# Kernel optimization log

Hardware: AMD Instinct MI355X
Metric: run time of the kernel (lower is better)

The kernel has to match this reference:

```python
import jax, jax.numpy as jnp
import numpy as np

N_NODES = 50000
N_EDGES = 600000
D_IN, D_HID, D_OUT = 128, 256, 128


def setup_inputs() -> dict:
    key = jax.random.key(0)
    ks = jax.random.split(key, 8)
    x = jax.random.normal(ks[0], (N_NODES, D_IN), dtype=jnp.float32)
    edge_index = jax.random.randint(ks[1], (2, N_EDGES), 0, N_NODES, dtype=jnp.int64)
    # init_method='uniform' -> edge_weights initialized to ones
    edge_weights = jnp.ones((N_EDGES,), dtype=jnp.float32)
    def lin(k, din, dout):
        s = 1.0 / np.sqrt(din)
        return jax.random.uniform(k, (din, dout), jnp.float32, -s, s)
    W1 = lin(ks[2], D_IN, D_HID)
    b1 = jnp.zeros((D_HID,), jnp.float32)
    W2 = lin(ks[3], D_HID, D_HID)
    b2 = jnp.zeros((D_HID,), jnp.float32)
    W3 = lin(ks[4], D_HID, D_OUT)
    b3 = jnp.zeros((D_OUT,), jnp.float32)
    return {"x": x, "edge_index": edge_index, "edge_weights": edge_weights,
            "W1": W1, "b1": b1, "W2": W2, "b2": b2, "W3": W3, "b3": b3}


def reference(x, edge_index, edge_weights, W1, b1, W2, b2, W3, b3):
    N = x.shape[0]
    # learnable metric: softplus on raw edge weights
    ew = jax.nn.softplus(edge_weights)
    src, dst = edge_index[0], edge_index[1]
    # GCNConv default: add self-loops with weight 1.0
    loop = jnp.arange(N, dtype=edge_index.dtype)
    s = jnp.concatenate([src, loop])
    d = jnp.concatenate([dst, loop])
    w = jnp.concatenate([ew, jnp.ones((N,), ew.dtype)])
    # symmetric degree normalization (gcn_norm); identical edge_weight across layers
    deg = jax.ops.segment_sum(w, d, num_segments=N)
    dinv = jnp.where(deg > 0, jax.lax.rsqrt(deg), jnp.zeros_like(deg))
    norm = dinv[s] * w * dinv[d]  # [E+N]

    def gcn_conv(h, W, b):
        h = h @ W                              # [N, dout]
        msg = h[s] * norm[:, None]             # gather + scale: [E+N, dout]
        out = jax.ops.segment_sum(msg, d, num_segments=N)  # scatter-add
        return out + b

    h = jax.nn.relu(gcn_conv(x, W1, b1))   # dropout p=0.0 -> identity
    h = jax.nn.relu(gcn_conv(h, W2, b2))
    return gcn_conv(h, W3, b3)
```

## Files before the change

kernel.cpp:

```cpp
#include <hip/hip_runtime.h>
#include <hip/hip_fp16.h>
#include <math.h>

#define N_NODES 50000
#define N_EDGES 600000
#define D_IN    128
#define D_HID   256
#define D_OUT   128
#define NB_SCAN ((N_NODES + 255) / 256)

typedef unsigned short u16;
typedef unsigned long long u64;
typedef __attribute__((ext_vector_type(8))) _Float16 f16x8;
typedef __attribute__((ext_vector_type(4))) float f32x4;
typedef __attribute__((ext_vector_type(2))) float f32x2v;
typedef __attribute__((ext_vector_type(4))) float f32x4v;
typedef __attribute__((ext_vector_type(2))) unsigned int u32x2v;
typedef __attribute__((ext_vector_type(2))) u16 u16x2v;
typedef __attribute__((ext_vector_type(4))) u16 u16x4v;

#define DC_SHIFT 44
#define DC_SCALE 1048576.0f
#define DC_MASK  ((1ULL << DC_SHIFT) - 1ULL)

__device__ __forceinline__ u16 f2h(float x) {
    __half h = __float2half_rn(x);
    return *reinterpret_cast<u16*>(&h);
}
__device__ __forceinline__ float h2f(u16 h) {
    __half hh = *reinterpret_cast<__half*>(&h);
    return __half2float(hh);
}
__device__ __forceinline__ float2 h2f2(unsigned int raw) {
    __half2 h = *reinterpret_cast<__half2*>(&raw);
    return __half22float2(h);
}
__device__ __forceinline__ int bcast_i(int v, int l) {
    return __builtin_amdgcn_readlane(v, l);
}
__device__ __forceinline__ float bcast_f(float v, int l) {
    return __int_as_float(__builtin_amdgcn_readlane(__float_as_int(v), l));
}


__global__ void k_hist(const int* __restrict__ dst, const float* __restrict__ w,
                       float* __restrict__ ew, int* __restrict__ rank,
                       u64* __restrict__ degcnt) {
    int e = blockIdx.x * blockDim.x + threadIdx.x;
    if (e >= N_EDGES) return;
    float x = w[e];
    float sp = fmaxf(x, 0.f) + log1pf(expf(-fabsf(x)));
    ew[e] = sp;
    int d = dst[e];
    u64 pack = (1ULL << DC_SHIFT) + (u64)__float2uint_rn(sp * DC_SCALE);
    u64 old = atomicAdd(&degcnt[d], pack);
    rank[e] = (int)(old >> DC_SHIFT);
}

__global__ void k_scan1(const u64* __restrict__ degcnt, int* __restrict__ rowptr,
                        int* __restrict__ bsum) {
    __shared__ int s[256];
    int b = blockIdx.x, t = threadIdx.x;
    int i = b * 256 + t;
    int v = (i < N_NODES) ? (int)(degcnt[i] >> DC_SHIFT) : 0;
    s[t] = v;
    __syncthreads();
    for (int off = 1; off < 256; off <<= 1) {
        int u = (t >= off) ? s[t - off] : 0;
        __syncthreads();
        s[t] += u;
        __syncthreads();
    }
    if (i < N_NODES) rowptr[i] = s[t] - v;
    if (t == 255) bsum[b] = s[255];
}

__global__ void k_scan23(const int* __restrict__ bsum, int* __restrict__ rowptr,
                         const u64* __restrict__ degcnt, float* __restrict__ dinv) {
    __shared__ int s[256];
    __shared__ int orig[256];
    int b = blockIdx.x, t = threadIdx.x;
    int v = (t < NB_SCAN) ? bsum[t] : 0;
    s[t] = v;
    orig[t] = v;
    __syncthreads();
    for (int off = 1; off < 256; off <<= 1) {
        int u = (t >= off) ? s[t - off] : 0;
        __syncthreads();
        s[t] += u;
        __syncthreads();
    }
    int boffb = s[b] - orig[b];
    int i = b * 256 + t;
    if (i < N_NODES) {
        rowptr[i] += boffb;
        float deg = (float)(degcnt[i] & DC_MASK) * (1.0f / DC_SCALE);
        dinv[i] = rsqrtf(1.0f + deg);
    }
    if (b == 0 && t == 0) rowptr[N_NODES] = s[NB_SCAN - 1];
}

__global__ void k_fill2(const int* __restrict__ src, const int* __restrict__ dst,
                        const float* __restrict__ ew, const int* __restrict__ rank,
                        const int* __restrict__ rowptr, const float* __restrict__ dinv,
                        int2* __restrict__ ecsr) {
    int e = blockIdx.x * blockDim.x + threadIdx.x;
    if (e >= N_EDGES) return;
    int s = src[e], d = dst[e];
    int pos = rowptr[d] + rank[e];
    float wfin = dinv[s] * ew[e] * dinv[d];
    ecsr[pos] = make_int2(s, __float_as_int(wfin));
}


#define WPREP_TOTAL 131072

__global__ void k_wprep(const float* __restrict__ W1, const float* __restrict__ W2,
                        const float* __restrict__ W3,
                        u16* __restrict__ B1, u16* __restrict__ B2, u16* __restrict__ B3) {
    int idx = blockIdx.x * blockDim.x + threadIdx.x;
    const float* W; u16* B; int K, N, base;
    if (idx < 32768)       { W = W1; B = B1; K = 128; N = 256; base = 0; }
    else if (idx < 98304)  { W = W2; B = B2; K = 256; N = 256; base = 32768; }
    else if (idx < 131072) { W = W3; B = B3; K = 256; N = 128; base = 98304; }
    else return;
    int p = idx - base;
    int n = p % N, k = p / N;
    float x = W[(size_t)k * N + n];
    u16 hi = f2h(x);
    u16 lo = f2h(x - h2f(hi));
    B[(size_t)n * (2 * K) + k] = hi;
    B[(size_t)n * (2 * K) + K + k] = lo;
}


template <int D, int INF, int OUTM, bool BIAS>
__global__ __launch_bounds__(256) void k_agg(const void* __restrict__ inv,
                                             const int* __restrict__ rowptr,
                                             const int2* __restrict__ ecsr,
                                             const float* __restrict__ dinv,
                                             const float* __restrict__ bias,
                                             void* __restrict__ outv) {
    int node = blockIdx.x * 4 + (threadIdx.x >> 6);
    int lane = threadIdx.x & 63;
    if (node >= N_NODES) return;
    float dn = dinv[node];
    float dd = dn * dn;
    int beg = rowptr[node], end = rowptr[node + 1];
    int deg = end - beg;
    int esrc = 0;
    float ewv = 0.f;
    if (lane < deg) {
        u32x2v t = __builtin_nontemporal_load(
            reinterpret_cast<const u32x2v*>(ecsr) + beg + lane);
        esrc = (int)t.x;
        ewv = __uint_as_float(t.y);
    }
    int dcap = (deg > 64) ? 64 : deg;

    if (D == 256) {
        const float* inf = (const float*)inv;
        const u16* inh = (const u16*)inv;
        float ax, ay, az, aw;
        if (INF == 0) {
            float4 sv = *(reinterpret_cast<const float4*>(inf + (size_t)node * D) + lane);
            ax = dd * sv.x; ay = dd * sv.y; az = dd * sv.z; aw = dd * sv.w;
        } else {
            uint2 raw = *reinterpret_cast<const uint2*>(inh + (size_t)node * D + lane * 4);
            float2 f01 = h2f2(raw.x), f23 = h2f2(raw.y);
            ax = dd * f01.x; ay = dd * f01.y; az = dd * f23.x; aw = dd * f23.y;
        }
        int j = 0;
        for (; j + 8 <= dcap; j += 8) {
            int si[8]; float wv[8];
            #pragma unroll
            for (int k = 0; k < 8; ++k) {
                si[k] = bcast_i(esrc, j + k);
                wv[k] = bcast_f(ewv, j + k);
            }
            if (INF == 0) {
                float4 r[8];
                #pragma unroll
                for (int k = 0; k < 8; ++k)
                    r[k] = *(reinterpret_cast<const float4*>(inf + (size_t)si[k] * D) + lane);
                #pragma unroll
                for (int k = 0; k < 8; ++k) {
                    ax += wv[k] * r[k].x; ay += wv[k] * r[k].y;
                    az += wv[k] * r[k].z; aw += wv[k] * r[k].w;
                }
            } else {
                uint2 q[8];
                #pragma unroll
                for (int k = 0; k < 8; ++k)
                    q[k] = *reinterpret_cast<const uint2*>(inh + (size_t)si[k] * D + lane * 4);
                #pragma unroll
                for (int k = 0; k < 8; ++k) {
                    float2 a = h2f2(q[k].x), b = h2f2(q[k].y);
                    ax += wv[k] * a.x; ay += wv[k] * a.y;
                    az += wv[k] * b.x; aw += wv[k] * b.y;
                }
            }
        }
        for (; j < dcap; ++j) {
            int s0 = bcast_i(esrc, j);
            float w0 = bcast_f(ewv, j);
            if (INF == 0) {
                float4 r0 = *(reinterpret_cast<const float4*>(inf + (size_t)s0 * D) + lane);
                ax += w0 * r0.x; ay += w0 * r0.y; az += w0 * r0.z; aw += w0 * r0.w;
            } else {
                uint2 q0 = *reinterpret_cast<const uint2*>(inh + (size_t)s0 * D + lane * 4);
                float2 a0 = h2f2(q0.x), b0 = h2f2(q0.y);
                ax += w0 * a0.x; ay += w0 * a0.y; az += w0 * b0.x; aw += w0 * b0.y;
            }
        }
        for (int p = beg + 64; p < end; ++p) {
            int2 e0 = ecsr[p];
            float w0 = __int_as_float(e0.y);
            if (INF == 0) {
                float4 r0 = *(reinterpret_cast<const float4*>(inf + (size_t)e0.x * D) + lane);
                ax += w0 * r0.x; ay += w0 * r0.y; az += w0 * r0.z; aw += w0 * r0.w;
            } else {
                uint2 q0 = *reinterpret_cast<const uint2*>(inh + (size_t)e0.x * D + lane * 4);
                float2 a0 = h2f2(q0.x), b0 = h2f2(q0.y);
                ax += w0 * a0.x; ay += w0 * a0.y; az += w0 * b0.x; aw += w0 * b0.y;
            }
        }
        if (OUTM == 0) {
            float* out = (float*)outv;
            if (BIAS) {
                float4 b = *(reinterpret_cast<const float4*>(bias) + lane);
                ax += b.x; ay += b.y; az += b.z; aw += b.w;
            }
            f32x4v res = {ax, ay, az, aw};
            __builtin_nontemporal_store(res,
                reinterpret_cast<f32x4v*>(out + (size_t)node * D) + lane);
        } else {
            u16* out = (u16*)outv;
            u16x4v hv = {f2h(ax), f2h(ay), f2h(az), f2h(aw)};
            __builtin_nontemporal_store(hv,
                reinterpret_cast<u16x4v*>(out + (size_t)node * D + lane * 4));
        }
    } else {
        const float* inf = (const float*)inv;
        const u16* inh = (const u16*)inv;
        float ax, ay;
        if (INF == 0) {
            float2 sv = *(reinterpret_cast<const float2*>(inf + (size_t)node * D) + lane);
            ax = dd * sv.x; ay = dd * sv.y;
        } else {
            unsigned int raw = *reinterpret_cast<const unsigned int*>(inh + (size_t)node * D + lane * 2);
            float2 f = h2f2(raw);
            ax = dd * f.x; ay = dd * f.y;
        }
        int j = 0;
        for (; j + 8 <= dcap; j += 8) {
            int si[8]; float wv[8];
            #pragma unroll
            for (int k = 0; k < 8; ++k) {
                si[k] = bcast_i(esrc, j + k);
                wv[k] = bcast_f(ewv, j + k);
            }
            if (INF == 0) {
                float2 r[8];
                #pragma unroll
                for (int k = 0; k < 8; ++k)
                    r[k] = *(reinterpret_cast<const float2*>(inf + (size_t)si[k] * D) + lane);
                #pragma unroll
                for (int k = 0; k < 8; ++k) {
                    ax += wv[k] * r[k].x; ay += wv[k] * r[k].y;
                }
            } else {
                unsigned int q[8];
                #pragma unroll
                for (int k = 0; k < 8; ++k)
                    q[k] = *reinterpret_cast<const unsigned int*>(inh + (size_t)si[k] * D + lane * 2);
                #pragma unroll
                for (int k = 0; k < 8; ++k) {
                    float2 f = h2f2(q[k]);
                    ax += wv[k] * f.x; ay += wv[k] * f.y;
                }
            }
        }
        for (; j < dcap; ++j) {
            int s0 = bcast_i(esrc, j);
            float w0 = bcast_f(ewv, j);
            if (INF == 0) {
                float2 r0 = *(reinterpret_cast<const float2*>(inf + (size_t)s0 * D) + lane);
                ax += w0 * r0.x; ay += w0 * r0.y;
            } else {
                unsigned int q0 = *reinterpret_cast<const unsigned int*>(inh + (size_t)s0 * D + lane * 2);
                float2 f0 = h2f2(q0);
                ax += w0 * f0.x; ay += w0 * f0.y;
            }
        }
        for (int p = beg + 64; p < end; ++p) {
            int2 e0 = ecsr[p];
            float w0 = __int_as_float(e0.y);
            if (INF == 0) {
                float2 r0 = *(reinterpret_cast<const float2*>(inf + (size_t)e0.x * D) + lane);
                ax += w0 * r0.x; ay += w0 * r0.y;
            } else {
                unsigned int q0 = *reinterpret_cast<const unsigned int*>(inh + (size_t)e0.x * D + lane * 2);
                float2 f0 = h2f2(q0);
                ax += w0 * f0.x; ay += w0 * f0.y;
            }
        }
        if (OUTM == 0) {
            float* out = (float*)outv;
            if (BIAS) {
                float2 b = *(reinterpret_cast<const float2*>(bias) + lane);
                ax += b.x; ay += b.y;
            }
            f32x2v res = {ax, ay};
            __builtin_nontemporal_store(res,
                reinterpret_cast<f32x2v*>(out + (size_t)node * D) + lane);
        } else {
            u16* out = (u16*)outv;
            u16x2v hv = {f2h(ax), f2h(ay)};
            __builtin_nontemporal_store(hv,
                reinterpret_cast<u16x2v*>(out + (size_t)node * D + lane * 2));
        }
    }
}


template <int OUT, bool BIAS, bool RELU>
__global__ __launch_bounds__(256) void k_gemm_h(const u16* __restrict__ Ap,
                                                const u16* __restrict__ Bp,
                                                const float* __restrict__ bias,
                                                void* __restrict__ Cv,
                                                int M, int K, int NN) {
    const int KP2 = 2 * K;
    __shared__ u16 As[8 * 544];
    __shared__ u16 Bs[2 * 8 * 544];
    int tid = threadIdx.x;
    int bm = blockIdx.y * 128;
    int bn = blockIdx.x * 128;
    int l = tid & 63;
    int w = tid >> 6;
    int wr = w >> 1, wc = w & 1;

    f32x4 zero = {0.f, 0.f, 0.f, 0.f};
    f32x4 acc[4][4];
    #pragma unroll
    for (int i = 0; i < 4; i++)
        #pragma unroll
        for (int j = 0; j < 4; j++) acc[i][j] = zero;

    for (int k0 = 0; k0 < K; k0 += 32) {
        #pragma unroll
        for (int q = 0; q < 2; q++) {
            int idx = tid + q * 256;
            int r = idx >> 2, o = idx & 3;
            int gr = bm + r;
            uint4 va = make_uint4(0u, 0u, 0u, 0u);
            if (gr < M)
                va = *reinterpret_cast<const uint4*>(Ap + (size_t)gr * K + k0 + o * 8);
            *reinterpret_cast<uint4*>(&As[(r >> 4) * 544 + o * 136 + (r & 15) * 8]) = va;
        }
        #pragma unroll
        for (int q = 0; q < 4; q++) {
            int idx = tid + q * 256;
            int r = idx >> 3, oct = idx & 7;
            int hf = oct >> 2, o = oct & 3;
            uint4 vb = *reinterpret_cast<const uint4*>(
                Bp + (size_t)(bn + r) * KP2 + hf * K + k0 + o * 8);
            *reinterpret_cast<uint4*>(
                &Bs[hf * 4352 + (r >> 4) * 544 + o * 136 + (r & 15) * 8]) = vb;
        }
        __syncthreads();
        int fro = (l >> 4) * 136 + (l & 15) * 8;
        f16x8 a[4], bh[4], bl[4];
        #pragma unroll
        for (int i = 0; i < 4; i++)
            a[i] = *reinterpret_cast<const f16x8*>(&As[(wr * 4 + i) * 544 + fro]);
        #pragma unroll
        for (int j = 0; j < 4; j++) {
            bh[j] = *reinterpret_cast<const f16x8*>(&Bs[(wc * 4 + j) * 544 + fro]);
            bl[j] = *reinterpret_cast<const f16x8*>(&Bs[4352 + (wc * 4 + j) * 544 + fro]);
        }
        #pragma unroll
        for (int i = 0; i < 4; i++)
            #pragma unroll
            for (int j = 0; j < 4; j++) {
                acc[i][j] = __builtin_amdgcn_mfma_f32_16x16x32_f16(a[i], bh[j], acc[i][j], 0, 0, 0);
                acc[i][j] = __builtin_amdgcn_mfma_f32_16x16x32_f16(a[i], bl[j], acc[i][j], 0, 0, 0);
            }
        __syncthreads();
    }

    int cl = l & 15;
    int rq = (l >> 4) * 4;
    float bv[4];
    #pragma unroll
    for (int j = 0; j < 4; j++) {
        int gc = bn + wc * 64 + j * 16 + cl;
        bv[j] = BIAS ? bias[gc] : 0.f;
    }
    #pragma unroll
    for (int i = 0; i < 4; i++) {
        #pragma unroll
        for (int r = 0; r < 4; r++) {
            int grow = bm + wr * 64 + i * 16 + rq + r;
            if (grow >= M) continue;
            #pragma unroll
            for (int j = 0; j < 4; j++) {
                int gc = bn + wc * 64 + j * 16 + cl;
                float v = acc[i][j][r];
                if (BIAS) v += bv[j];
                if (RELU) v = fmaxf(v, 0.f);
                if (OUT == 0) {
                    ((float*)Cv)[(size_t)grow * NN + gc] = v;
                } else {
                    ((u16*)Cv)[(size_t)grow * NN + gc] = f2h(v);
                }
            }
        }
    }
}


extern "C" void kernel_launch(void* const* d_in, const int* in_sizes, int n_in,
                              void* d_out, int out_size, void* d_ws, size_t ws_size,
                              hipStream_t stream) {
    const float* x   = (const float*)d_in[0];
    const int*   ei  = (const int*)d_in[1];
    const float* wts = (const float*)d_in[2];
    const float* W1  = (const float*)d_in[3];
    const float* b1  = (const float*)d_in[4];
    const float* W2  = (const float*)d_in[5];
    const float* b2  = (const float*)d_in[6];
    const float* W3  = (const float*)d_in[7];
    const float* b3  = (const float*)d_in[8];
    float* out = (float*)d_out;
    const int* src = ei;
    const int* dst = ei + N_EDGES;

    float* bufA   = (float*)d_ws;
    float* bufB   = bufA + (size_t)N_NODES * D_HID;
    float* ew     = bufB + (size_t)N_NODES * D_HID;
    float* dinv   = ew + N_EDGES;
    int*   cnt    = (int*)(dinv + N_NODES);
    int*   rank   = cnt + N_NODES;
    int*   rowptr = rank + N_EDGES;
    int2*  ecsr   = (int2*)(rowptr + (N_NODES + 2));
    u16*   Wb1    = (u16*)(ecsr + N_EDGES);
    u16*   Wb2    = Wb1 + 256 * 256;
    u16*   Wb3    = Wb2 + 256 * 512;
    int*   bsum   = (int*)(Wb3 + 128 * 512);
    u64*   degcnt = (u64*)bufB;

    (void)hipMemsetAsync(degcnt, 0, sizeof(u64) * N_NODES, stream);

    int ethreads = 256;
    int eblocks = (N_EDGES + ethreads - 1) / ethreads;
    k_hist<<<eblocks, ethreads, 0, stream>>>(dst, wts, ew, rank, degcnt);
    k_scan1<<<NB_SCAN, 256, 0, stream>>>(degcnt, rowptr, bsum);
    k_scan23<<<NB_SCAN, 256, 0, stream>>>(bsum, rowptr, degcnt, dinv);
    k_fill2<<<eblocks, ethreads, 0, stream>>>(src, dst, ew, rank, rowptr, dinv, ecsr);
    k_wprep<<<(WPREP_TOTAL + 255) / 256, 256, 0, stream>>>(W1, W2, W3, Wb1, Wb2, Wb3);

    int aggBlocks = (N_NODES + 3) / 4;
    int gy = (N_NODES + 127) / 128;

    k_agg<128, 0, 1, false><<<aggBlocks, 256, 0, stream>>>(x, rowptr, ecsr, dinv, nullptr, bufA);
    {
        dim3 g(2, gy);
        k_gemm_h<1, true, true><<<g, 256, 0, stream>>>((const u16*)bufA, Wb1, b1, bufB,
                                                       N_NODES, D_IN, D_HID);
    }
    k_agg<256, 1, 1, false><<<aggBlocks, 256, 0, stream>>>(bufB, rowptr, ecsr, dinv, nullptr, bufA);
    {
        dim3 g(2, gy);
        k_gemm_h<1, true, true><<<g, 256, 0, stream>>>((const u16*)bufA, Wb2, b2, bufB,
                                                       N_NODES, D_HID, D_HID);
    }
    {
        dim3 g(1, gy);
        k_gemm_h<1, false, false><<<g, 256, 0, stream>>>((const u16*)bufB, Wb3, nullptr, bufA,
                                                         N_NODES, D_HID, D_OUT);
    }
    k_agg<128, 1, 0, true><<<aggBlocks, 256, 0, stream>>>(bufA, rowptr, ecsr, dinv, b3, out);
}
```

Measured before the change: 337.5 us.

## Fuse graph setup kernels into one persistent kernel with grid barriers

Replaces the memset, histogram, two scan kernels, CSR fill and weight-prep launches with a single persistent kernel of fixed block count that moves between phases through a software grid-wide barrier. The intent is to remove several kernel launch gaps and the separate memset. In exchange, the edge loops now run grid-stride over fewer threads, and the design relies on all 512 blocks being resident at once to avoid deadlock. Each barrier also costs a global atomic round trip.

```diff
diff --git a/kernel.cpp b/kernel.cpp
--- a/kernel.cpp
+++ b/kernel.cpp
@@ -8,6 +8,9 @@
 #define D_HID   256
 #define D_OUT   128
 #define NB_SCAN ((N_NODES + 255) / 256)
+
+#define SETUP_BLOCKS 512
+#define SETUP_THREADS (SETUP_BLOCKS * 256)
 
 typedef unsigned short u16;
 typedef unsigned long long u64;
@@ -23,6 +26,8 @@
 #define DC_SCALE 1048576.0f
 #define DC_MASK  ((1ULL << DC_SHIFT) - 1ULL)
 
+#define WPREP_TOTAL 131072
+
 __device__ __forceinline__ u16 f2h(float x) {
     __half h = __float2half_rn(x);
     return *reinterpret_cast<u16*>(&h);
@@ -42,95 +47,114 @@
     return __int_as_float(__builtin_amdgcn_readlane(__float_as_int(v), l));
 }
 
-
-__global__ void k_hist(const int* __restrict__ dst, const float* __restrict__ w,
-                       float* __restrict__ ew, int* __restrict__ rank,
-                       u64* __restrict__ degcnt) {
-    int e = blockIdx.x * blockDim.x + threadIdx.x;
-    if (e >= N_EDGES) return;
-    float x = w[e];
-    float sp = fmaxf(x, 0.f) + log1pf(expf(-fabsf(x)));
-    ew[e] = sp;
-    int d = dst[e];
-    u64 pack = (1ULL << DC_SHIFT) + (u64)__float2uint_rn(sp * DC_SCALE);
-    u64 old = atomicAdd(&degcnt[d], pack);
-    rank[e] = (int)(old >> DC_SHIFT);
-}
-
-__global__ void k_scan1(const u64* __restrict__ degcnt, int* __restrict__ rowptr,
-                        int* __restrict__ bsum) {
-    __shared__ int s[256];
-    int b = blockIdx.x, t = threadIdx.x;
-    int i = b * 256 + t;
-    int v = (i < N_NODES) ? (int)(degcnt[i] >> DC_SHIFT) : 0;
-    s[t] = v;
+__device__ __forceinline__ void grid_barrier(int* __restrict__ bar) {
     __syncthreads();
-    for (int off = 1; off < 256; off <<= 1) {
-        int u = (t >= off) ? s[t - off] : 0;
-        __syncthreads();
-        s[t] += u;
-        __syncthreads();
-    }
-    if (i < N_NODES) rowptr[i] = s[t] - v;
-    if (t == 255) bsum[b] = s[255];
-}
-
-__global__ void k_scan23(const int* __restrict__ bsum, int* __restrict__ rowptr,
-                         const u64* __restrict__ degcnt, float* __restrict__ dinv) {
+    if (threadIdx.x == 0) {
+        __threadfence();
+        int g0 = __hip_atomic_load(&bar[1], __ATOMIC_ACQUIRE, __HIP_MEMORY_SCOPE_AGENT);
+        int old = __hip_atomic_fetch_add(&bar[0], 1, __ATOMIC_ACQ_REL, __HIP_MEMORY_SCOPE_AGENT);
+        if (old == SETUP_BLOCKS - 1) {
+            __hip_atomic_store(&bar[0], 0, __ATOMIC_RELAXED, __HIP_MEMORY_SCOPE_AGENT);
+            __hip_atomic_fetch_add(&bar[1], 1, __ATOMIC_RELEASE, __HIP_MEMORY_SCOPE_AGENT);
+        } else {
+            while (__hip_atomic_load(&bar[1], __ATOMIC_ACQUIRE, __HIP_MEMORY_SCOPE_AGENT) == g0)
+                __builtin_amdgcn_s_sleep(2);
+        }
+    }
+    __syncthreads();
+}
+
+__global__ __launch_bounds__(256, 4) void k_setup(
+        const int* __restrict__ src, const int* __restrict__ dst,
+        const float* __restrict__ wts,
+        float* __restrict__ ew, int* __restrict__ rank,
+        u64* __restrict__ degcnt, int* __restrict__ rowptr,
+        int* __restrict__ bsum, float* __restrict__ dinv,
+        int2* __restrict__ ecsr,
+        const float* __restrict__ W1, const float* __restrict__ W2,
+        const float* __restrict__ W3,
+        u16* __restrict__ B1, u16* __restrict__ B2, u16* __restrict__ B3,
+        int* __restrict__ bar) {
     __shared__ int s[256];
     __shared__ int orig[256];
     int b = blockIdx.x, t = threadIdx.x;
-    int v = (t < NB_SCAN) ? bsum[t] : 0;
-    s[t] = v;
-    orig[t] = v;
-    __syncthreads();
-    for (int off = 1; off < 256; off <<= 1) {
-        int u = (t >= off) ? s[t - off] : 0;
+    int gid = b * 256 + t;
+
+    for (int g = gid; g < N_NODES + WPREP_TOTAL; g += SETUP_THREADS) {
+        if (g < N_NODES) {
+            degcnt[g] = 0ULL;
+        } else {
+            int idx = g - N_NODES;
+            const float* W; u16* B; int K, N, base;
+            if (idx < 32768)      { W = W1; B = B1; K = 128; N = 256; base = 0; }
+            else if (idx < 98304) { W = W2; B = B2; K = 256; N = 256; base = 32768; }
+            else                  { W = W3; B = B3; K = 256; N = 128; base = 98304; }
+            int p = idx - base;
+            int n = p % N, k = p / N;
+            float x = W[(size_t)k * N + n];
+            u16 hi = f2h(x);
+            u16 lo = f2h(x - h2f(hi));
+            B[(size_t)n * (2 * K) + k] = hi;
+            B[(size_t)n * (2 * K) + K + k] = lo;
+        }
+    }
+    grid_barrier(bar);
+
+    for (int e = gid; e < N_EDGES; e += SETUP_THREADS) {
+        float x = wts[e];
+        float sp = fmaxf(x, 0.f) + log1pf(expf(-fabsf(x)));
+        ew[e] = sp;
+        int d = dst[e];
+        u64 pack = (1ULL << DC_SHIFT) + (u64)__float2uint_rn(sp * DC_SCALE);
+        u64 old = atomicAdd(&degcnt[d], pack);
+        rank[e] = (int)(old >> DC_SHIFT);
+    }
+    grid_barrier(bar);
+
+    if (b < NB_SCAN) {
+        int i = b * 256 + t;
+        int v = (i < N_NODES) ? (int)(degcnt[i] >> DC_SHIFT) : 0;
+        s[t] = v;
         __syncthreads();
-        s[t] += u;
+        for (int off = 1; off < 256; off <<= 1) {
+            int u = (t >= off) ? s[t - off] : 0;
+            __syncthreads();
+            s[t] += u;
+            __syncthreads();
+        }
+        if (i < N_NODES) rowptr[i] = s[t] - v;
+        if (t == 255) bsum[b] = s[255];
+    }
+    grid_barrier(bar);
+
+    if (b < NB_SCAN) {
+        int v = (t < NB_SCAN) ? bsum[t] : 0;
+        s[t] = v;
+        orig[t] = v;
         __syncthreads();
-    }
-    int boffb = s[b] - orig[b];
-    int i = b * 256 + t;
-    if (i < N_NODES) {
-        rowptr[i] += boffb;
-        float deg = (float)(degcnt[i] & DC_MASK) * (1.0f / DC_SCALE);
-        dinv[i] = rsqrtf(1.0f + deg);
-    }
-    if (b == 0 && t == 0) rowptr[N_NODES] = s[NB_SCAN - 1];
-}
-
-__global__ void k_fill2(const int* __restrict__ src, const int* __restrict__ dst,
-                        const float* __restrict__ ew, const int* __restrict__ rank,
-                        const int* __restrict__ rowptr, const float* __restrict__ dinv,
-                        int2* __restrict__ ecsr) {
-    int e = blockIdx.x * blockDim.x + threadIdx.x;
-    if (e >= N_EDGES) return;
-    int s = src[e], d = dst[e];
-    int pos = rowptr[d] + rank[e];
-    float wfin = dinv[s] * ew[e] * dinv[d];
-    ecsr[pos] = make_int2(s, __float_as_int(wfin));
-}
-
-
-#define WPREP_TOTAL 131072
-
-__global__ void k_wprep(const float* __restrict__ W1, const float* __restrict__ W2,
-                        const float* __restrict__ W3,
-                        u16* __restrict__ B1, u16* __restrict__ B2, u16* __restrict__ B3) {
-    int idx = blockIdx.x * blockDim.x + threadIdx.x;
-    const float* W; u16* B; int K, N, base;
-    if (idx < 32768)       { W = W1; B = B1; K = 128; N = 256; base = 0; }
-    else if (idx < 98304)  { W = W2; B = B2; K = 256; N = 256; base = 32768; }
-    else if (idx < 131072) { W = W3; B = B3; K = 256; N = 128; base = 98304; }
-    else return;
-    int p = idx - base;
-    int n = p % N, k = p / N;
-    float x = W[(size_t)k * N + n];
-    u16 hi = f2h(x);
-    u16 lo = f2h(x - h2f(hi));
-    B[(size_t)n * (2 * K) + k] = hi;
-    B[(size_t)n * (2 * K) + K + k] = lo;
+        for (int off = 1; off < 256; off <<= 1) {
+            int u = (t >= off) ? s[t - off] : 0;
+            __syncthreads();
+            s[t] += u;
+            __syncthreads();
+        }
+        int boffb = s[b] - orig[b];
+        int i = b * 256 + t;
+        if (i < N_NODES) {
+            rowptr[i] += boffb;
+            float deg = (float)(degcnt[i] & DC_MASK) * (1.0f / DC_SCALE);
+            dinv[i] = rsqrtf(1.0f + deg);
+        }
+        if (b == 0 && t == 0) rowptr[N_NODES] = s[NB_SCAN - 1];
+    }
+    grid_barrier(bar);
+
+    for (int e = gid; e < N_EDGES; e += SETUP_THREADS) {
+        int ss = src[e], d = dst[e];
+        int pos = rowptr[d] + rank[e];
+        float wfin = dinv[ss] * ew[e] * dinv[d];
+        ecsr[pos] = make_int2(ss, __float_as_int(wfin));
+    }
 }
 
 
@@ -448,17 +472,14 @@
     u16*   Wb2    = Wb1 + 256 * 256;
     u16*   Wb3    = Wb2 + 256 * 512;
     int*   bsum   = (int*)(Wb3 + 128 * 512);
+    int*   bar    = bsum + NB_SCAN + 2;
     u64*   degcnt = (u64*)bufB;
 
-    (void)hipMemsetAsync(degcnt, 0, sizeof(u64) * N_NODES, stream);
-
-    int ethreads = 256;
-    int eblocks = (N_EDGES + ethreads - 1) / ethreads;
-    k_hist<<<eblocks, ethreads, 0, stream>>>(dst, wts, ew, rank, degcnt);
-    k_scan1<<<NB_SCAN, 256, 0, stream>>>(degcnt, rowptr, bsum);
-    k_scan23<<<NB_SCAN, 256, 0, stream>>>(bsum, rowptr, degcnt, dinv);
-    k_fill2<<<eblocks, ethreads, 0, stream>>>(src, dst, ew, rank, rowptr, dinv, ecsr);
-    k_wprep<<<(WPREP_TOTAL + 255) / 256, 256, 0, stream>>>(W1, W2, W3, Wb1, Wb2, Wb3);
+    (void)hipMemsetAsync(bar, 0, sizeof(int) * 2, stream);
+
+    k_setup<<<SETUP_BLOCKS, 256, 0, stream>>>(
+        src, dst, wts, ew, rank, degcnt, rowptr, bsum, dinv, ecsr,
+        W1, W2, W3, Wb1, Wb2, Wb3, bar);
 
     int aggBlocks = (N_NODES + 3) / 4;
     int gy = (N_NODES + 127) / 128;
```

Measured after the change: 596.6 us. 1.77x slower.

## Fuse edge histogram, weight prep and fp16 input cast into one setup kernel

Applied to the files above, without the earlier changes.

Merges the degree-histogram kernel and the weight hi/lo split into a single grid-stride setup kernel, which also casts the input features to fp16 ahead of time. The first aggregation then gathers fp16 rows instead of fp32 rows, halving the bytes moved by its irregular neighbour gathers. The scan reads only the upper 32-bit word of each packed degree counter. In exchange, the input is rounded to fp16 before the first aggregation rather than after it, which slightly changes numerics, and the cast adds a full extra pass over x.

```diff
diff --git a/kernel.cpp b/kernel.cpp
--- a/kernel.cpp
+++ b/kernel.cpp
@@ -23,6 +23,9 @@
 #define DC_SCALE 1048576.0f
 #define DC_MASK  ((1ULL << DC_SHIFT) - 1ULL)
 
+#define WPREP_TOTAL 131072
+#define CAST_TOTAL  (N_NODES * 32)
+
 __device__ __forceinline__ u16 f2h(float x) {
     __half h = __float2half_rn(x);
     return *reinterpret_cast<u16*>(&h);
@@ -42,19 +45,44 @@
     return __int_as_float(__builtin_amdgcn_readlane(__float_as_int(v), l));
 }
 
-
-__global__ void k_hist(const int* __restrict__ dst, const float* __restrict__ w,
-                       float* __restrict__ ew, int* __restrict__ rank,
-                       u64* __restrict__ degcnt) {
-    int e = blockIdx.x * blockDim.x + threadIdx.x;
-    if (e >= N_EDGES) return;
-    float x = w[e];
-    float sp = fmaxf(x, 0.f) + log1pf(expf(-fabsf(x)));
-    ew[e] = sp;
-    int d = dst[e];
-    u64 pack = (1ULL << DC_SHIFT) + (u64)__float2uint_rn(sp * DC_SCALE);
-    u64 old = atomicAdd(&degcnt[d], pack);
-    rank[e] = (int)(old >> DC_SHIFT);
+__global__ __launch_bounds__(256) void k_setup0(
+        const int* __restrict__ dst, const float* __restrict__ wts,
+        float* __restrict__ ew, int* __restrict__ rank,
+        u64* __restrict__ degcnt,
+        const float* __restrict__ x, u16* __restrict__ xh,
+        const float* __restrict__ W1, const float* __restrict__ W2,
+        const float* __restrict__ W3,
+        u16* __restrict__ B1, u16* __restrict__ B2, u16* __restrict__ B3) {
+    int gid = blockIdx.x * blockDim.x + threadIdx.x;
+    int stride = gridDim.x * blockDim.x;
+
+    for (int e = gid; e < N_EDGES; e += stride) {
+        float v = wts[e];
+        float sp = fmaxf(v, 0.f) + log1pf(expf(-fabsf(v)));
+        ew[e] = sp;
+        int d = dst[e];
+        u64 pack = (1ULL << DC_SHIFT) + (u64)__float2uint_rn(sp * DC_SCALE);
+        u64 old = atomicAdd(&degcnt[d], pack);
+        rank[e] = (int)(old >> DC_SHIFT);
+    }
+    for (int g = gid; g < CAST_TOTAL; g += stride) {
+        float4 v = reinterpret_cast<const float4*>(x)[g];
+        u16x4v h = {f2h(v.x), f2h(v.y), f2h(v.z), f2h(v.w)};
+        reinterpret_cast<u16x4v*>(xh)[g] = h;
+    }
+    for (int g = gid; g < WPREP_TOTAL; g += stride) {
+        const float* W; u16* B; int K, N, base;
+        if (g < 32768)      { W = W1; B = B1; K = 128; N = 256; base = 0; }
+        else if (g < 98304) { W = W2; B = B2; K = 256; N = 256; base = 32768; }
+        else                { W = W3; B = B3; K = 256; N = 128; base = 98304; }
+        int p = g - base;
+        int n = p % N, k = p / N;
+        float v = W[(size_t)k * N + n];
+        u16 hi = f2h(v);
+        u16 lo = f2h(v - h2f(hi));
+        B[(size_t)n * (2 * K) + k] = hi;
+        B[(size_t)n * (2 * K) + K + k] = lo;
+    }
 }
 
 __global__ void k_scan1(const u64* __restrict__ degcnt, int* __restrict__ rowptr,
@@ -62,7 +90,9 @@
     __shared__ int s[256];
     int b = blockIdx.x, t = threadIdx.x;
     int i = b * 256 + t;
-    int v = (i < N_NODES) ? (int)(degcnt[i] >> DC_SHIFT) : 0;
+    int v = (i < N_NODES)
+          ? (int)(reinterpret_cast<const unsigned int*>(degcnt)[2 * i + 1] >> (DC_SHIFT - 32))
+          : 0;
     s[t] = v;
     __syncthreads();
     for (int off = 1; off < 256; off <<= 1) {
@@ -110,27 +140,6 @@
     int pos = rowptr[d] + rank[e];
     float wfin = dinv[s] * ew[e] * dinv[d];
     ecsr[pos] = make_int2(s, __float_as_int(wfin));
-}
-
-
-#define WPREP_TOTAL 131072
-
-__global__ void k_wprep(const float* __restrict__ W1, const float* __restrict__ W2,
-                        const float* __restrict__ W3,
-                        u16* __restrict__ B1, u16* __restrict__ B2, u16* __restrict__ B3) {
-    int idx = blockIdx.x * blockDim.x + threadIdx.x;
-    const float* W; u16* B; int K, N, base;
-    if (idx < 32768)       { W = W1; B = B1; K = 128; N = 256; base = 0; }
-    else if (idx < 98304)  { W = W2; B = B2; K = 256; N = 256; base = 32768; }
-    else if (idx < 131072) { W = W3; B = B3; K = 256; N = 128; base = 98304; }
-    else return;
-    int p = idx - base;
-    int n = p % N, k = p / N;
-    float x = W[(size_t)k * N + n];
-    u16 hi = f2h(x);
-    u16 lo = f2h(x - h2f(hi));
-    B[(size_t)n * (2 * K) + k] = hi;
-    B[(size_t)n * (2 * K) + K + k] = lo;
 }
 
 
@@ -449,21 +458,22 @@
     u16*   Wb3    = Wb2 + 256 * 512;
     int*   bsum   = (int*)(Wb3 + 128 * 512);
     u64*   degcnt = (u64*)bufB;
+    u16*   xh     = (u16*)(bufB + (size_t)N_NODES * D_HID / 2);
 
     (void)hipMemsetAsync(degcnt, 0, sizeof(u64) * N_NODES, stream);
 
     int ethreads = 256;
     int eblocks = (N_EDGES + ethreads - 1) / ethreads;
-    k_hist<<<eblocks, ethreads, 0, stream>>>(dst, wts, ew, rank, degcnt);
+    k_setup0<<<eblocks, ethreads, 0, stream>>>(dst, wts, ew, rank, degcnt,
+                                               x, xh, W1, W2, W3, Wb1, Wb2, Wb3);
     k_scan1<<<NB_SCAN, 256, 0, stream>>>(degcnt, rowptr, bsum);
     k_scan23<<<NB_SCAN, 256, 0, stream>>>(bsum, rowptr, degcnt, dinv);
     k_fill2<<<eblocks, ethreads, 0, stream>>>(src, dst, ew, rank, rowptr, dinv, ecsr);
-    k_wprep<<<(WPREP_TOTAL + 255) / 256, 256, 0, stream>>>(W1, W2, W3, Wb1, Wb2, Wb3);
 
     int aggBlocks = (N_NODES + 3) / 4;
     int gy = (N_NODES + 127) / 128;
 
-    k_agg<128, 0, 1, false><<<aggBlocks, 256, 0, stream>>>(x, rowptr, ecsr, dinv, nullptr, bufA);
+    k_agg<128, 1, 1, false><<<aggBlocks, 256, 0, stream>>>(xh, rowptr, ecsr, dinv, nullptr, bufA);
     {
         dim3 g(2, gy);
         k_gemm_h<1, true, true><<<g, 256, 0, stream>>>((const u16*)bufA, Wb1, b1, bufB,
```

New measurement: 329.3 us. 1.02x faster.
